# Optimization experiments

Measured on AMD Instinct MI355X. Metric: run time of the kernel, lower is better.

## Reference

```python
import jax, jax.numpy as jnp
import numpy as np

N_USER, N_MOVIE, H, E = 100000, 50000, 512, 500000

def setup_inputs() -> dict:
    key = jax.random.key(0)
    ks = jax.random.split(key, 8)
    z_user = jax.random.normal(ks[0], (N_USER, H), dtype=jnp.float32)
    z_movie = jax.random.normal(ks[1], (N_MOVIE, H), dtype=jnp.float32)
    edge_row = jax.random.randint(ks[2], (E,), 0, N_USER, dtype=jnp.int64)
    edge_col = jax.random.randint(ks[3], (E,), 0, N_MOVIE, dtype=jnp.int64)
    w1 = jax.random.normal(ks[4], (2 * H, H), dtype=jnp.float32) * (1.0 / np.sqrt(2 * H))
    b1 = jax.random.normal(ks[5], (H,), dtype=jnp.float32) * 0.01
    w2 = jax.random.normal(ks[6], (H, 1), dtype=jnp.float32) * (1.0 / np.sqrt(H))
    b2 = jax.random.normal(ks[7], (1,), dtype=jnp.float32) * 0.01
    return {"z_user": z_user, "z_movie": z_movie, "edge_row": edge_row,
            "edge_col": edge_col, "w1": w1, "b1": b1, "w2": w2, "b2": b2}

def reference(z_user, z_movie, edge_row, edge_col, w1, b1, w2, b2):
    # Gather endpoint embeddings and concat -> [E, 2H]
    z = jnp.concatenate([z_user[edge_row], z_movie[edge_col]], axis=-1)
    h = jax.nn.relu(z @ w1 + b1)      # [E, H]
    out = h @ w2 + b2                 # [E, 1]
    return out.reshape(-1)
```

## Files before the change

### kernel.cpp

```cpp
#include <hip/hip_runtime.h>
#include <hip/hip_bf16.h>

typedef __attribute__((ext_vector_type(8))) short bf16x8;
typedef __attribute__((ext_vector_type(4))) float f32x4;

#define HDIM 512
#define BM 128
#define BN 128
#define BK 64
#define BKP 72

__device__ __forceinline__ unsigned short f2bf(float f) {
  unsigned u = __float_as_uint(f);
  u += 0x7fffu + ((u >> 16) & 1u);
  return (unsigned short)(u >> 16);
}

__global__ void k_w1t(const float* __restrict__ w1, unsigned short* __restrict__ w1t) {
  int idx = blockIdx.x * 256 + threadIdx.x;
  int k = idx >> 9;
  int n = idx & 511;
  w1t[n * 1024 + k] = f2bf(w1[idx]);
}

__global__ __launch_bounds__(256) void k_gemm(const float* __restrict__ A, int M,
    const unsigned short* __restrict__ w1t, int koff,
    unsigned short* __restrict__ C)
{
  __shared__ unsigned short As[BM][BKP];
  __shared__ unsigned short Bs[BN][BKP];
  const int tid  = threadIdx.x;
  const int lane = tid & 63;
  const int wid  = tid >> 6;
  const int wm = wid >> 1, wn = wid & 1;
  const int lm = lane & 15, lq = lane >> 4;
  const int mbase = blockIdx.x * BM;
  const int nbase = blockIdx.y * BN;

  f32x4 acc[4][4];
  #pragma unroll
  for (int i = 0; i < 4; ++i)
    #pragma unroll
    for (int j = 0; j < 4; ++j) acc[i][j] = (f32x4){0.f, 0.f, 0.f, 0.f};

  for (int kb = 0; kb < HDIM / BK; ++kb) {
    const int k0 = kb * BK;
    __syncthreads();
    #pragma unroll
    for (int i = 0; i < 8; ++i) {
      int fid = i * 256 + tid;
      int r = fid >> 4, c4 = fid & 15;
      int row = mbase + r; if (row > M - 1) row = M - 1;
      const float4 v = *(const float4*)&A[(size_t)row * HDIM + k0 + c4 * 4];
      ushort4 o; o.x = f2bf(v.x); o.y = f2bf(v.y); o.z = f2bf(v.z); o.w = f2bf(v.w);
      *(ushort4*)&As[r][c4 * 4] = o;
    }
    #pragma unroll
    for (int i = 0; i < 4; ++i) {
      int cid = i * 256 + tid;
      int r = cid >> 3, c8 = cid & 7;
      const ushort4* g = (const ushort4*)&w1t[(size_t)(nbase + r) * 1024 + koff + k0 + c8 * 8];
      ushort4 lo = g[0], hi = g[1];
      *(ushort4*)&Bs[r][c8 * 8]     = lo;
      *(ushort4*)&Bs[r][c8 * 8 + 4] = hi;
    }
    __syncthreads();
    #pragma unroll
    for (int ks = 0; ks < 2; ++ks) {
      bf16x8 af[4], bfr[4];
      #pragma unroll
      for (int t = 0; t < 4; ++t) {
        af[t]  = *(const bf16x8*)&As[wm * 64 + t * 16 + lm][ks * 32 + lq * 8];
        bfr[t] = *(const bf16x8*)&Bs[wn * 64 + t * 16 + lm][ks * 32 + lq * 8];
      }
      #pragma unroll
      for (int mi = 0; mi < 4; ++mi)
        #pragma unroll
        for (int ni = 0; ni < 4; ++ni)
          acc[mi][ni] = __builtin_amdgcn_mfma_f32_16x16x32_bf16(af[mi], bfr[ni], acc[mi][ni], 0, 0, 0);
    }
  }
  #pragma unroll
  for (int mi = 0; mi < 4; ++mi)
    #pragma unroll
    for (int ni = 0; ni < 4; ++ni)
      #pragma unroll
      for (int r = 0; r < 4; ++r) {
        int rg = mbase + wm * 64 + mi * 16 + lq * 4 + r;
        int cg = nbase + wn * 64 + ni * 16 + lm;
        if (rg < M) C[(size_t)rg * HDIM + cg] = f2bf(acc[mi][ni][r]);
      }
}

__global__ __launch_bounds__(256) void k_edge(const int* __restrict__ er, const int* __restrict__ ec,
    const unsigned short* __restrict__ u1, const unsigned short* __restrict__ m1,
    const float* __restrict__ b1, const float* __restrict__ w2, const float* __restrict__ b2,
    float* __restrict__ out, int E)
{
  const int lane = threadIdx.x & 63;
  const int gwid = blockIdx.x * 4 + (threadIdx.x >> 6);
  const int nw   = gridDim.x * 4;
  const float4 b1a = *(const float4*)&b1[lane * 8];
  const float4 b1b = *(const float4*)&b1[lane * 8 + 4];
  const float4 w2a = *(const float4*)&w2[lane * 8];
  const float4 w2b = *(const float4*)&w2[lane * 8 + 4];
  const float bias2 = b2[0];
  for (int e = gwid; e < E; e += nw) {
    const int r = er[e], c = ec[e];
    const uint4 ua = *(const uint4*)&u1[(size_t)r * HDIM + lane * 8];
    const uint4 va = *(const uint4*)&m1[(size_t)c * HDIM + lane * 8];
    float p = 0.f, s;
    s = __uint_as_float(ua.x << 16)        + __uint_as_float(va.x << 16)        + b1a.x; s = fmaxf(s, 0.f); p += s * w2a.x;
    s = __uint_as_float(ua.x & 0xffff0000u)+ __uint_as_float(va.x & 0xffff0000u)+ b1a.y; s = fmaxf(s, 0.f); p += s * w2a.y;
    s = __uint_as_float(ua.y << 16)        + __uint_as_float(va.y << 16)        + b1a.z; s = fmaxf(s, 0.f); p += s * w2a.z;
    s = __uint_as_float(ua.y & 0xffff0000u)+ __uint_as_float(va.y & 0xffff0000u)+ b1a.w; s = fmaxf(s, 0.f); p += s * w2a.w;
    s = __uint_as_float(ua.z << 16)        + __uint_as_float(va.z << 16)        + b1b.x; s = fmaxf(s, 0.f); p += s * w2b.x;
    s = __uint_as_float(ua.z & 0xffff0000u)+ __uint_as_float(va.z & 0xffff0000u)+ b1b.y; s = fmaxf(s, 0.f); p += s * w2b.y;
    s = __uint_as_float(ua.w << 16)        + __uint_as_float(va.w << 16)        + b1b.z; s = fmaxf(s, 0.f); p += s * w2b.z;
    s = __uint_as_float(ua.w & 0xffff0000u)+ __uint_as_float(va.w & 0xffff0000u)+ b1b.w; s = fmaxf(s, 0.f); p += s * w2b.w;
    #pragma unroll
    for (int off = 32; off > 0; off >>= 1) p += __shfl_down(p, off, 64);
    if (lane == 0) out[e] = p + bias2;
  }
}

__global__ __launch_bounds__(256) void k_fallback(const float* __restrict__ zu, const float* __restrict__ zm,
    const int* __restrict__ er, const int* __restrict__ ec, const float* __restrict__ w1,
    const float* __restrict__ b1, const float* __restrict__ w2, const float* __restrict__ b2,
    float* __restrict__ out, int E)
{
  __shared__ float Zs[64][33];
  __shared__ float Ws[32][65];
  __shared__ float outacc[64];
  __shared__ int ridx[64], cidx[64];
  const int tid = threadIdx.x;
  const int ebase = blockIdx.x * 64;
  if (tid < 64) {
    int e = ebase + tid; if (e > E - 1) e = E - 1;
    ridx[tid] = er[e]; cidx[tid] = ec[e];
    outacc[tid] = 0.f;
  }
  const int tx = tid & 15, ty = tid >> 4;
  for (int nt = 0; nt < 8; ++nt) {
    float acc[4][4] = {};
    for (int kc = 0; kc < 32; ++kc) {
      __syncthreads();
      #pragma unroll
      for (int i = 0; i < 8; ++i) {
        int id = i * 256 + tid;
        int rr = id >> 5, cc = id & 31;
        int k = kc * 32 + cc;
        Zs[rr][cc] = (k < 512) ? zu[(size_t)ridx[rr] * 512 + k]
                               : zm[(size_t)cidx[rr] * 512 + (k - 512)];
      }
      #pragma unroll
      for (int i = 0; i < 8; ++i) {
        int id = i * 256 + tid;
        int kk = id >> 6, nn = id & 63;
        Ws[kk][nn] = w1[(size_t)(kc * 32 + kk) * 512 + nt * 64 + nn];
      }
      __syncthreads();
      #pragma unroll
      for (int kk = 0; kk < 32; ++kk) {
        float a0 = Zs[ty*4+0][kk], a1 = Zs[ty*4+1][kk], a2 = Zs[ty*4+2][kk], a3 = Zs[ty*4+3][kk];
        float q0 = Ws[kk][tx*4+0], q1 = Ws[kk][tx*4+1], q2 = Ws[kk][tx*4+2], q3 = Ws[kk][tx*4+3];
        acc[0][0] += a0*q0; acc[0][1] += a0*q1; acc[0][2] += a0*q2; acc[0][3] += a0*q3;
        acc[1][0] += a1*q0; acc[1][1] += a1*q1; acc[1][2] += a1*q2; acc[1][3] += a1*q3;
        acc[2][0] += a2*q0; acc[2][1] += a2*q1; acc[2][2] += a2*q2; acc[2][3] += a2*q3;
        acc[3][0] += a3*q0; acc[3][1] += a3*q1; acc[3][2] += a3*q2; acc[3][3] += a3*q3;
      }
    }
    #pragma unroll
    for (int i = 0; i < 4; ++i) {
      float p = 0.f;
      #pragma unroll
      for (int j = 0; j < 4; ++j) {
        int n = nt * 64 + tx * 4 + j;
        float h = acc[i][j] + b1[n]; h = fmaxf(h, 0.f);
        p += h * w2[n];
      }
      atomicAdd(&outacc[ty * 4 + i], p);
    }
  }
  __syncthreads();
  if (tid < 64 && (ebase + tid) < E) out[ebase + tid] = outacc[tid] + b2[0];
}

extern "C" void kernel_launch(void* const* d_in, const int* in_sizes, int n_in,
                              void* d_out, int out_size, void* d_ws, size_t ws_size,
                              hipStream_t stream)
{
  const float* z_user  = (const float*)d_in[0];
  const float* z_movie = (const float*)d_in[1];
  const int*   erow    = (const int*)d_in[2];
  const int*   ecol    = (const int*)d_in[3];
  const float* w1      = (const float*)d_in[4];
  const float* b1      = (const float*)d_in[5];
  const float* w2      = (const float*)d_in[6];
  const float* b2      = (const float*)d_in[7];
  float* out = (float*)d_out;

  const int NU = in_sizes[0] / HDIM;
  const int NM = in_sizes[1] / HDIM;
  const int E  = in_sizes[2];

  const size_t need = ((size_t)NU * HDIM + (size_t)NM * HDIM + (size_t)1024 * 512) * 2;
  if (ws_size >= need) {
    unsigned short* u1  = (unsigned short*)d_ws;
    unsigned short* m1  = u1 + (size_t)NU * HDIM;
    unsigned short* w1t = m1 + (size_t)NM * HDIM;
    k_w1t<<<(1024 * 512) / 256, 256, 0, stream>>>(w1, w1t);
    k_gemm<<<dim3((NU + BM - 1) / BM, HDIM / BN), 256, 0, stream>>>(z_user,  NU, w1t, 0,   u1);
    k_gemm<<<dim3((NM + BM - 1) / BM, HDIM / BN), 256, 0, stream>>>(z_movie, NM, w1t, 512, m1);
    k_edge<<<2048, 256, 0, stream>>>(erow, ecol, u1, m1, b1, w2, b2, out, E);
  } else {
    k_fallback<<<(E + 63) / 64, 256, 0, stream>>>(z_user, z_movie, erow, ecol, w1, b1, w2, b2, out, E);
  }
}
```

Measured before the change: 656.2 us.

## Widen GEMM N-tile, reorder grid for A reuse, batch two edges per wave

The projection GEMM now uses 256-wide N tiles with 512 threads, so each fp32 A row-block is fetched and converted for 2 N-blocks instead of 4. The grid is reordered so blocks sharing the same A rows run next to each other, which helps L2 reuse. The conversion to bf16 now uses packed intrinsics, and B is loaded with 16-byte vectors. The edge kernel handles two edges per wave to put more gathers in flight and share the shuffle reduction, but this assumes E is even and adds register pressure.

```diff
diff --git a/kernel.cpp b/kernel.cpp
--- a/kernel.cpp
+++ b/kernel.cpp
@@ -6,7 +6,7 @@
 
 #define HDIM 512
 #define BM 128
-#define BN 128
+#define BN 256
 #define BK 64
 #define BKP 72
 
@@ -14,6 +14,12 @@
   unsigned u = __float_as_uint(f);
   u += 0x7fffu + ((u >> 16) & 1u);
   return (unsigned short)(u >> 16);
+}
+
+__device__ __forceinline__ unsigned int pk_bf(float x, float y) {
+  __hip_bfloat162 h = __float22bfloat162_rn(float2{x, y});
+  union { __hip_bfloat162 b; unsigned int u; } cv; cv.b = h;
+  return cv.u;
 }
 
 __global__ void k_w1t(const float* __restrict__ w1, unsigned short* __restrict__ w1t) {
@@ -23,7 +29,7 @@
   w1t[n * 1024 + k] = f2bf(w1[idx]);
 }
 
-__global__ __launch_bounds__(256) void k_gemm(const float* __restrict__ A, int M,
+__global__ __launch_bounds__(512) void k_gemm(const float* __restrict__ A, int M,
     const unsigned short* __restrict__ w1t, int koff,
     unsigned short* __restrict__ C)
 {
@@ -32,10 +38,10 @@
   const int tid  = threadIdx.x;
   const int lane = tid & 63;
   const int wid  = tid >> 6;
-  const int wm = wid >> 1, wn = wid & 1;
+  const int wm = wid & 1, wn = wid >> 1;
   const int lm = lane & 15, lq = lane >> 4;
-  const int mbase = blockIdx.x * BM;
-  const int nbase = blockIdx.y * BN;
+  const int nbase = blockIdx.x * BN;
+  const int mbase = blockIdx.y * BM;
 
   f32x4 acc[4][4];
   #pragma unroll
@@ -47,22 +53,21 @@
     const int k0 = kb * BK;
     __syncthreads();
     #pragma unroll
-    for (int i = 0; i < 8; ++i) {
-      int fid = i * 256 + tid;
+    for (int i = 0; i < 4; ++i) {
+      int fid = i * 512 + tid;
       int r = fid >> 4, c4 = fid & 15;
       int row = mbase + r; if (row > M - 1) row = M - 1;
       const float4 v = *(const float4*)&A[(size_t)row * HDIM + k0 + c4 * 4];
-      ushort4 o; o.x = f2bf(v.x); o.y = f2bf(v.y); o.z = f2bf(v.z); o.w = f2bf(v.w);
-      *(ushort4*)&As[r][c4 * 4] = o;
+      unsigned int* dst = (unsigned int*)&As[r][c4 * 4];
+      dst[0] = pk_bf(v.x, v.y);
+      dst[1] = pk_bf(v.z, v.w);
     }
     #pragma unroll
     for (int i = 0; i < 4; ++i) {
-      int cid = i * 256 + tid;
+      int cid = i * 512 + tid;
       int r = cid >> 3, c8 = cid & 7;
-      const ushort4* g = (const ushort4*)&w1t[(size_t)(nbase + r) * 1024 + koff + k0 + c8 * 8];
-      ushort4 lo = g[0], hi = g[1];
-      *(ushort4*)&Bs[r][c8 * 8]     = lo;
-      *(ushort4*)&Bs[r][c8 * 8 + 4] = hi;
+      const bf16x8 g = *(const bf16x8*)&w1t[(size_t)(nbase + r) * 1024 + koff + k0 + c8 * 8];
+      *(bf16x8*)&Bs[r][c8 * 8] = g;
     }
     __syncthreads();
     #pragma unroll
@@ -105,22 +110,36 @@
   const float4 w2a = *(const float4*)&w2[lane * 8];
   const float4 w2b = *(const float4*)&w2[lane * 8 + 4];
   const float bias2 = b2[0];
-  for (int e = gwid; e < E; e += nw) {
-    const int r = er[e], c = ec[e];
-    const uint4 ua = *(const uint4*)&u1[(size_t)r * HDIM + lane * 8];
-    const uint4 va = *(const uint4*)&m1[(size_t)c * HDIM + lane * 8];
-    float p = 0.f, s;
-    s = __uint_as_float(ua.x << 16)        + __uint_as_float(va.x << 16)        + b1a.x; s = fmaxf(s, 0.f); p += s * w2a.x;
-    s = __uint_as_float(ua.x & 0xffff0000u)+ __uint_as_float(va.x & 0xffff0000u)+ b1a.y; s = fmaxf(s, 0.f); p += s * w2a.y;
-    s = __uint_as_float(ua.y << 16)        + __uint_as_float(va.y << 16)        + b1a.z; s = fmaxf(s, 0.f); p += s * w2a.z;
-    s = __uint_as_float(ua.y & 0xffff0000u)+ __uint_as_float(va.y & 0xffff0000u)+ b1a.w; s = fmaxf(s, 0.f); p += s * w2a.w;
-    s = __uint_as_float(ua.z << 16)        + __uint_as_float(va.z << 16)        + b1b.x; s = fmaxf(s, 0.f); p += s * w2b.x;
-    s = __uint_as_float(ua.z & 0xffff0000u)+ __uint_as_float(va.z & 0xffff0000u)+ b1b.y; s = fmaxf(s, 0.f); p += s * w2b.y;
-    s = __uint_as_float(ua.w << 16)        + __uint_as_float(va.w << 16)        + b1b.z; s = fmaxf(s, 0.f); p += s * w2b.z;
-    s = __uint_as_float(ua.w & 0xffff0000u)+ __uint_as_float(va.w & 0xffff0000u)+ b1b.w; s = fmaxf(s, 0.f); p += s * w2b.w;
-    #pragma unroll
-    for (int off = 32; off > 0; off >>= 1) p += __shfl_down(p, off, 64);
-    if (lane == 0) out[e] = p + bias2;
+  for (int e = gwid * 2; e < E; e += nw * 2) {
+    const int r0 = er[e], c0 = ec[e];
+    const int r1 = er[e + 1], c1 = ec[e + 1];
+    const uint4 ua0 = *(const uint4*)&u1[(size_t)r0 * HDIM + lane * 8];
+    const uint4 va0 = *(const uint4*)&m1[(size_t)c0 * HDIM + lane * 8];
+    const uint4 ua1 = *(const uint4*)&u1[(size_t)r1 * HDIM + lane * 8];
+    const uint4 va1 = *(const uint4*)&m1[(size_t)c1 * HDIM + lane * 8];
+    float p0 = 0.f, p1 = 0.f, s;
+    s = __uint_as_float(ua0.x << 16)        + __uint_as_float(va0.x << 16)        + b1a.x; s = fmaxf(s, 0.f); p0 += s * w2a.x;
+    s = __uint_as_float(ua0.x & 0xffff0000u)+ __uint_as_float(va0.x & 0xffff0000u)+ b1a.y; s = fmaxf(s, 0.f); p0 += s * w2a.y;
+    s = __uint_as_float(ua0.y << 16)        + __uint_as_float(va0.y << 16)        + b1a.z; s = fmaxf(s, 0.f); p0 += s * w2a.z;
+    s = __uint_as_float(ua0.y & 0xffff0000u)+ __uint_as_float(va0.y & 0xffff0000u)+ b1a.w; s = fmaxf(s, 0.f); p0 += s * w2a.w;
+    s = __uint_as_float(ua0.z << 16)        + __uint_as_float(va0.z << 16)        + b1b.x; s = fmaxf(s, 0.f); p0 += s * w2b.x;
+    s = __uint_as_float(ua0.z & 0xffff0000u)+ __uint_as_float(va0.z & 0xffff0000u)+ b1b.y; s = fmaxf(s, 0.f); p0 += s * w2b.y;
+    s = __uint_as_float(ua0.w << 16)        + __uint_as_float(va0.w << 16)        + b1b.z; s = fmaxf(s, 0.f); p0 += s * w2b.z;
+    s = __uint_as_float(ua0.w & 0xffff0000u)+ __uint_as_float(va0.w & 0xffff0000u)+ b1b.w; s = fmaxf(s, 0.f); p0 += s * w2b.w;
+    s = __uint_as_float(ua1.x << 16)        + __uint_as_float(va1.x << 16)        + b1a.x; s = fmaxf(s, 0.f); p1 += s * w2a.x;
+    s = __uint_as_float(ua1.x & 0xffff0000u)+ __uint_as_float(va1.x & 0xffff0000u)+ b1a.y; s = fmaxf(s, 0.f); p1 += s * w2a.y;
+    s = __uint_as_float(ua1.y << 16)        + __uint_as_float(va1.y << 16)        + b1a.z; s = fmaxf(s, 0.f); p1 += s * w2a.z;
+    s = __uint_as_float(ua1.y & 0xffff0000u)+ __uint_as_float(va1.y & 0xffff0000u)+ b1a.w; s = fmaxf(s, 0.f); p1 += s * w2a.w;
+    s = __uint_as_float(ua1.z << 16)        + __uint_as_float(va1.z << 16)        + b1b.x; s = fmaxf(s, 0.f); p1 += s * w2b.x;
+    s = __uint_as_float(ua1.z & 0xffff0000u)+ __uint_as_float(va1.z & 0xffff0000u)+ b1b.y; s = fmaxf(s, 0.f); p1 += s * w2b.y;
+    s = __uint_as_float(ua1.w << 16)        + __uint_as_float(va1.w << 16)        + b1b.z; s = fmaxf(s, 0.f); p1 += s * w2b.z;
+    s = __uint_as_float(ua1.w & 0xffff0000u)+ __uint_as_float(va1.w & 0xffff0000u)+ b1b.w; s = fmaxf(s, 0.f); p1 += s * w2b.w;
+    #pragma unroll
+    for (int off = 32; off > 0; off >>= 1) {
+      p0 += __shfl_down(p0, off, 64);
+      p1 += __shfl_down(p1, off, 64);
+    }
+    if (lane == 0) *(float2*)&out[e] = float2{p0 + bias2, p1 + bias2};
   }
 }
 
@@ -210,8 +229,8 @@
     unsigned short* m1  = u1 + (size_t)NU * HDIM;
     unsigned short* w1t = m1 + (size_t)NM * HDIM;
     k_w1t<<<(1024 * 512) / 256, 256, 0, stream>>>(w1, w1t);
-    k_gemm<<<dim3((NU + BM - 1) / BM, HDIM / BN), 256, 0, stream>>>(z_user,  NU, w1t, 0,   u1);
-    k_gemm<<<dim3((NM + BM - 1) / BM, HDIM / BN), 256, 0, stream>>>(z_movie, NM, w1t, 512, m1);
+    k_gemm<<<dim3(HDIM / BN, (NU + BM - 1) / BM), 512, 0, stream>>>(z_user,  NU, w1t, 0,   u1);
+    k_gemm<<<dim3(HDIM / BN, (NM + BM - 1) / BM), 512, 0, stream>>>(z_movie, NM, w1t, 512, m1);
     k_edge<<<2048, 256, 0, stream>>>(erow, ecol, u1, m1, b1, w2, b2, out, E);
   } else {
     k_fallback<<<(E + 63) / 64, 256, 0, stream>>>(z_user, z_movie, erow, ecol, w1, b1, w2, b2, out, E);
```

Result: faster. 594.6 us (-9.4%).
